# Optimization experiments

Measured on AMD Instinct MI355X. Metric: run time of the kernel, lower is better.

The kernel has to match this reference:

```python
import jax, jax.numpy as jnp
import numpy as np
from functools import partial

T, N, E, F_IN, H, F_OUT, L = 12, 20000, 320000, 128, 256, 128, 2


def _agg(feat, src, dst, n):
    # copy_u('x','m') + sum('m','h_N'): for each dst node, sum src-node features
    return jax.ops.segment_sum(feat[src], dst, num_segments=n)


def setup_inputs() -> dict:
    key = jax.random.key(0)
    ks = jax.random.split(key, 16)
    sc = 0.05
    inp = {
        "x": jax.random.normal(ks[0], (T, N, F_IN), jnp.float32),
        "h0": jax.random.normal(ks[1], (L, N, H), jnp.float32),
        "src": jax.random.randint(ks[2], (E,), 0, N, jnp.int32),
        "dst": jax.random.randint(ks[3], (E,), 0, N, jnp.int32),
        # layer 0: x-nets map F_IN->H, h-nets map H->H; stacked [r, u, c]
        "Wx0": jax.random.normal(ks[4], (3, F_IN, H), jnp.float32) * sc,
        "bx0": jnp.zeros((3, H), jnp.float32),
        "Wh0": jax.random.normal(ks[5], (3, H, H), jnp.float32) * sc,
        "bh0": jnp.zeros((3, H), jnp.float32),
        # layer 1: both map H->H
        "Wx1": jax.random.normal(ks[6], (3, H, H), jnp.float32) * sc,
        "bx1": jnp.zeros((3, H), jnp.float32),
        "Wh1": jax.random.normal(ks[7], (3, H, H), jnp.float32) * sc,
        "bh1": jnp.zeros((3, H), jnp.float32),
        "Wo": jax.random.normal(ks[8], (H, F_OUT), jnp.float32) * sc,
        "bo": jnp.zeros((F_OUT,), jnp.float32),
    }
    return inp


def _gru_cell(x_agg, h, Wx, bx, Wh, bh, src, dst, n):
    # reuse_msg_passing=True: h_agg computed once, shared by r_h_net and u_h_net
    h_agg = _agg(h, src, dst, n)
    r = jax.nn.sigmoid(x_agg @ Wx[0] + bx[0] + h_agg @ Wh[0] + bh[0])
    u = jax.nn.sigmoid(x_agg @ Wx[1] + bx[1] + h_agg @ Wh[1] + bh[1])
    # c_h_net runs on r*h, so it needs its own aggregation
    c = jnp.tanh(x_agg @ Wx[2] + bx[2] + _agg(r * h, src, dst, n) @ Wh[2] + bh[2])
    return u * h + (1.0 - u) * c


def reference(x, h0, src, dst, Wx0, bx0, Wh0, bh0, Wx1, bx1, Wh1, bh1, Wo, bo):
    n = h0.shape[1]
    # merge_time_steps=True: aggregate all time steps of x in one pass
    x_aggs = jax.vmap(lambda xi: _agg(xi, src, dst, n))(x)  # [T, N, F_IN]

    def step(carry, x_agg_t):
        h_0, h_1 = carry
        nh0 = _gru_cell(x_agg_t, h_0, Wx0, bx0, Wh0, bh0, src, dst, n)
        nh1 = _gru_cell(_agg(nh0, src, dst, n), h_1, Wx1, bx1, Wh1, bh1, src, dst, n)
        return (nh0, nh1), nh1 @ Wo + bo

    (hf0, hf1), outputs = jax.lax.scan(step, (h0[0], h0[1]), x_aggs)
    return outputs, jnp.stack([hf0, hf1])  # [T,N,F_OUT], [L,N,H]
```

## Files before the change

kernel.cpp:

```cpp
#include <hip/hip_runtime.h>
#include <hip/hip_bf16.h>
#include <stdint.h>

#define T_STEPS 12
#define NN 20000
#define NE 320000
#define FIN 128
#define HD 256
#define FOUT 128
#define PADR 96

typedef __attribute__((ext_vector_type(4))) float f32x4;
typedef __attribute__((ext_vector_type(8))) _Float16 f16x8;

static __device__ __forceinline__ float sigmoidf_(float x) {
  return 1.0f / (1.0f + __expf(-x));
}
static __device__ __forceinline__ ushort f2h(float f) {
  union { ushort s; _Float16 h; } v; v.h = (_Float16)f; return v.s;
}

static __device__ __forceinline__ void gload_lds16(const _Float16* g, _Float16* l) {
  auto gp = (const __attribute__((address_space(1))) _Float16*)g;
  auto lp = (__attribute__((address_space(3))) _Float16*)l;
  __builtin_amdgcn_global_load_lds(gp, lp, 16, 0, 0);
}

__global__ void count_kernel(const int* __restrict__ dst, int* __restrict__ counts) {
  int e = blockIdx.x * blockDim.x + threadIdx.x;
  if (e < NE) atomicAdd(&counts[dst[e]], 1);
}

__global__ void scan_kernel(const int* __restrict__ counts, int* __restrict__ offs,
                            int* __restrict__ cursor) {
  __shared__ int sm[1024];
  __shared__ int carry_s;
  if (threadIdx.x == 0) carry_s = 0;
  __syncthreads();
  const int n = NN;
  int nch = (n + 1023) >> 10;
  for (int c = 0; c < nch; ++c) {
    int i = (c << 10) + (int)threadIdx.x;
    int v = (i < n) ? counts[i] : 0;
    sm[threadIdx.x] = v;
    __syncthreads();
    for (int off = 1; off < 1024; off <<= 1) {
      int t = (threadIdx.x >= (unsigned)off) ? sm[threadIdx.x - off] : 0;
      __syncthreads();
      sm[threadIdx.x] += t;
      __syncthreads();
    }
    int incl = sm[threadIdx.x];
    int carry_local = carry_s;
    if (i < n) {
      int excl = carry_local + incl - v;
      offs[i] = excl;
      cursor[i] = excl;
    }
    __syncthreads();
    if (threadIdx.x == 1023) carry_s = carry_local + incl;
    __syncthreads();
  }
  if (threadIdx.x == 0) offs[n] = carry_s;
}

__global__ void fill_kernel(const int* __restrict__ src, const int* __restrict__ dst,
                            int* __restrict__ cursor, int* __restrict__ esrc) {
  int e = blockIdx.x * blockDim.x + threadIdx.x;
  if (e < NE) {
    int d = dst[e];
    int pos = atomicAdd(&cursor[d], 1);
    esrc[pos] = src[e];
  }
}

static __device__ __forceinline__ void agg_body256(int blk, const float* __restrict__ feat,
                                                   const int* __restrict__ offs,
                                                   const int* __restrict__ esrc,
                                                   _Float16* __restrict__ out) {
  int d = blk * 4 + (threadIdx.x >> 6);
  int lane = threadIdx.x & 63;
  int beg = offs[d], end = offs[d + 1];
  float a[8][4] = {};
  int e = beg;
  for (; e + 7 < end; e += 8) {
#pragma unroll
    for (int u = 0; u < 8; ++u) {
      float4 v = *reinterpret_cast<const float4*>(feat + (size_t)esrc[e + u] * 256 + lane * 4);
      a[u][0] += v.x; a[u][1] += v.y; a[u][2] += v.z; a[u][3] += v.w;
    }
  }
  for (; e + 3 < end; e += 4) {
#pragma unroll
    for (int u = 0; u < 4; ++u) {
      float4 v = *reinterpret_cast<const float4*>(feat + (size_t)esrc[e + u] * 256 + lane * 4);
      a[u][0] += v.x; a[u][1] += v.y; a[u][2] += v.z; a[u][3] += v.w;
    }
  }
  for (; e < end; ++e) {
    float4 v = *reinterpret_cast<const float4*>(feat + (size_t)esrc[e] * 256 + lane * 4);
    a[0][0] += v.x; a[0][1] += v.y; a[0][2] += v.z; a[0][3] += v.w;
  }
  ushort hi[4], lo[4];
#pragma unroll
  for (int p = 0; p < 4; ++p) {
    float s = ((a[0][p] + a[1][p]) + (a[2][p] + a[3][p])) +
              ((a[4][p] + a[5][p]) + (a[6][p] + a[7][p]));
    hi[p] = f2h(s);
    union { ushort us; _Float16 h; } u; u.us = hi[p];
    lo[p] = f2h(s - (float)u.h);
  }
  *reinterpret_cast<ushort4*>(out + (size_t)d * 512 + lane * 4) = *reinterpret_cast<ushort4*>(hi);
  *reinterpret_cast<ushort4*>(out + (size_t)d * 512 + 256 + lane * 4) = *reinterpret_cast<ushort4*>(lo);
}

__global__ void agg_split_h(const float* __restrict__ feat, const int* __restrict__ offs,
                            const int* __restrict__ esrc, _Float16* __restrict__ out) {
  agg_body256(blockIdx.x, feat, offs, esrc, out);
}

__global__ void agg_dual(const float* __restrict__ f0, _Float16* __restrict__ o0,
                         const float* __restrict__ f1, _Float16* __restrict__ o1,
                         const int* __restrict__ offs, const int* __restrict__ esrc) {
  if (blockIdx.y == 0) agg_body256(blockIdx.x, f0, offs, esrc, o0);
  else                 agg_body256(blockIdx.x, f1, offs, esrc, o1);
}

__global__ void agg_split_x(const float* __restrict__ x, const int* __restrict__ offs,
                            const int* __restrict__ esrc, _Float16* __restrict__ out) {
  int t = blockIdx.y;
  const float* feat = x + (size_t)t * NN * FIN;
  _Float16* o = out + (size_t)t * NN * 256;
  int d = blockIdx.x * 4 + (threadIdx.x >> 6);
  int lane = threadIdx.x & 63;
  int beg = offs[d], end = offs[d + 1];
  float a[8][2] = {};
  int e = beg;
  for (; e + 7 < end; e += 8) {
#pragma unroll
    for (int u = 0; u < 8; ++u) {
      float2 v = *reinterpret_cast<const float2*>(feat + (size_t)esrc[e + u] * FIN + lane * 2);
      a[u][0] += v.x; a[u][1] += v.y;
    }
  }
  for (; e + 3 < end; e += 4) {
#pragma unroll
    for (int u = 0; u < 4; ++u) {
      float2 v = *reinterpret_cast<const float2*>(feat + (size_t)esrc[e + u] * FIN + lane * 2);
      a[u][0] += v.x; a[u][1] += v.y;
    }
  }
  for (; e < end; ++e) {
    float2 v = *reinterpret_cast<const float2*>(feat + (size_t)esrc[e] * FIN + lane * 2);
    a[0][0] += v.x; a[0][1] += v.y;
  }
  float s0 = ((a[0][0] + a[1][0]) + (a[2][0] + a[3][0])) +
             ((a[4][0] + a[5][0]) + (a[6][0] + a[7][0]));
  float s1 = ((a[0][1] + a[1][1]) + (a[2][1] + a[3][1])) +
             ((a[4][1] + a[5][1]) + (a[6][1] + a[7][1]));
  ushort2 hi, lo;
  hi.x = f2h(s0); hi.y = f2h(s1);
  union { ushort s; _Float16 h; } u0, u1;
  u0.s = hi.x; u1.s = hi.y;
  lo.x = f2h(s0 - (float)u0.h); lo.y = f2h(s1 - (float)u1.h);
  *reinterpret_cast<ushort2*>(o + (size_t)d * 256 + lane * 2) = hi;
  *reinterpret_cast<ushort2*>(o + (size_t)d * 256 + FIN + lane * 2) = lo;
}

struct GemmP {
  const _Float16* Aa; int lda_a, wrapA, lenA;
  const _Float16* Ab; int lda_b, wrapB;
  const _Float16* B; int ldb;
  float* C; int ldc;
  const float* bias;
  const float* Cacc;
  int M, K, mode;
  float* h; _Float16* hf; float* rh;
  int nch, rpg;
};

static __device__ __forceinline__ void gemm_body(int p, const GemmP& g,
                                                 _Float16* As, _Float16* Bs) {
  int xcd = p & 7;
  int q = p >> 3;
  int rowt = xcd * g.rpg + q / g.nch;
  int chunk = q % g.nch;
  int m0 = rowt * 128;
  if (m0 >= g.M) return;
  int n0 = chunk * 128;

  int tid = threadIdx.x;
  int wave = tid >> 6;
  int lane = tid & 63;
  int wm = wave >> 1, wn = wave & 1;
  int lrow = lane & 15;
  int kgrp = lane >> 4;

  f32x4 acc[4][4] = {};

  int row8 = lane >> 3;
  int swz8 = 8 * ((lane & 7) ^ row8);
  int wrow = wave * 32;

  for (int k0 = 0; k0 < g.K; k0 += 64) {
    const _Float16* Abase;
    int ka, ldA;
    if (k0 < g.lenA) {
      ka = (k0 >= g.wrapA) ? k0 - g.wrapA : k0;
      Abase = g.Aa; ldA = g.lda_a;
    } else {
      int kp = k0 - g.lenA;
      ka = (kp >= g.wrapB) ? kp - g.wrapB : kp;
      Abase = g.Ab; ldA = g.lda_b;
    }
    __syncthreads();
#pragma unroll
    for (int p4 = 0; p4 < 4; ++p4) {
      int r = wrow + p4 * 8;
      gload_lds16(&Abase[(size_t)(m0 + r + row8) * ldA + ka + swz8], &As[r * 64]);
      gload_lds16(&g.B[(size_t)(n0 + r + row8) * g.ldb + k0 + swz8], &Bs[r * 64]);
    }
    __syncthreads();

#pragma unroll
    for (int kk = 0; kk < 2; ++kk) {
      f16x8 af[4], bf[4];
      int kbyte = kk * 64 + kgrp * 16;
#pragma unroll
      for (int i = 0; i < 4; ++i) {
        int ar = wm * 64 + i * 16 + lrow;
        af[i] = *reinterpret_cast<const f16x8*>(
            reinterpret_cast<const char*>(As) + ar * 128 + (kbyte ^ ((ar & 7) << 4)));
        int br = wn * 64 + i * 16 + lrow;
        bf[i] = *reinterpret_cast<const f16x8*>(
            reinterpret_cast<const char*>(Bs) + br * 128 + (kbyte ^ ((br & 7) << 4)));
      }
#pragma unroll
      for (int i = 0; i < 4; ++i)
#pragma unroll
        for (int j = 0; j < 4; ++j)
          acc[i][j] = __builtin_amdgcn_mfma_f32_16x16x32_f16(bf[j], af[i], acc[i][j], 0, 0, 0);
    }
  }

#pragma unroll
  for (int i = 0; i < 4; ++i) {
    int m = m0 + wm * 64 + i * 16 + lrow;
    if (m >= g.M) continue;
#pragma unroll
    for (int j = 0; j < 4; ++j) {
      int colbase = n0 + wn * 64 + j * 16 + kgrp * 4;
      f32x4 v = acc[i][j];
      if (g.mode == 0) {
        float4 bv4 = *reinterpret_cast<const float4*>(&g.bias[colbase]);
        v[0] += bv4.x; v[1] += bv4.y; v[2] += bv4.z; v[3] += bv4.w;
        *reinterpret_cast<f32x4*>(&g.C[(size_t)m * g.ldc + colbase]) = v;
      } else if (g.mode == 1) {
        if (g.Cacc) {
          float4 a4 = *reinterpret_cast<const float4*>(&g.Cacc[(size_t)m * g.ldc + colbase]);
          v[0] += a4.x; v[1] += a4.y; v[2] += a4.z; v[3] += a4.w;
        } else {
          float4 bv4 = *reinterpret_cast<const float4*>(&g.bias[colbase]);
          v[0] += bv4.x; v[1] += bv4.y; v[2] += bv4.z; v[3] += bv4.w;
        }
        if (colbase < 256) {
          float4 hv = *reinterpret_cast<const float4*>(&g.h[(size_t)m * 256 + colbase]);
          f32x4 rv;
          rv[0] = sigmoidf_(v[0]) * hv.x;
          rv[1] = sigmoidf_(v[1]) * hv.y;
          rv[2] = sigmoidf_(v[2]) * hv.z;
          rv[3] = sigmoidf_(v[3]) * hv.w;
          *reinterpret_cast<f32x4*>(&g.rh[(size_t)m * 256 + colbase]) = rv;
        } else if (colbase < 512) {
          v[0] = sigmoidf_(v[0]); v[1] = sigmoidf_(v[1]);
          v[2] = sigmoidf_(v[2]); v[3] = sigmoidf_(v[3]);
          *reinterpret_cast<f32x4*>(&g.C[(size_t)m * g.ldc + colbase]) = v;
        } else {
          *reinterpret_cast<f32x4*>(&g.C[(size_t)m * g.ldc + colbase]) = v;
        }
      } else {
        float4 xc = *reinterpret_cast<const float4*>(&g.C[(size_t)m * g.ldc + 512 + colbase]);
        float4 uu = *reinterpret_cast<const float4*>(&g.C[(size_t)m * g.ldc + 256 + colbase]);
        float* hp = &g.h[(size_t)m * 256 + colbase];
        float4 hv = *reinterpret_cast<const float4*>(hp);
        float4 nh;
        nh.x = uu.x * hv.x + (1.f - uu.x) * tanhf(xc.x + v[0]);
        nh.y = uu.y * hv.y + (1.f - uu.y) * tanhf(xc.y + v[1]);
        nh.z = uu.z * hv.z + (1.f - uu.z) * tanhf(xc.z + v[2]);
        nh.w = uu.w * hv.w + (1.f - uu.w) * tanhf(xc.w + v[3]);
        *reinterpret_cast<float4*>(hp) = nh;
        if (g.hf) {
          ushort4 hv16;
          hv16.x = f2h(nh.x); hv16.y = f2h(nh.y);
          hv16.z = f2h(nh.z); hv16.w = f2h(nh.w);
          *reinterpret_cast<ushort4*>(&g.hf[(size_t)m * 256 + colbase]) = hv16;
        }
      }
    }
  }
}

__global__ __launch_bounds__(256) void combo(GemmP ga, int na, GemmP gb, int nb, GemmP gc) {
  __shared__ _Float16 As[128 * 64];
  __shared__ _Float16 Bs[128 * 64];
  int b = blockIdx.x;
  int sel = (b < na) ? 0 : ((b < na + nb) ? 1 : 2);
  int idx = b - ((sel > 0) ? na : 0) - ((sel > 1) ? nb : 0);
  GemmP g = (sel == 0) ? ga : ((sel == 1) ? gb : gc);
  gemm_body(idx, g, As, Bs);
}

__global__ void wtrans(const float* __restrict__ W, _Float16* __restrict__ dst,
                       int K, int ldw, int ldd, int koff, int mode) {
  int k = blockIdx.x * blockDim.x + threadIdx.x;
  int n = blockIdx.y;
  if (k < K) {
    float w = W[(size_t)k * ldw + n];
    _Float16 hi = (_Float16)w;
    dst[(size_t)n * ldd + koff + k] = mode ? (_Float16)(w - (float)hi) : hi;
  }
}

__global__ void bias_comb(const float* __restrict__ bx, const float* __restrict__ bh,
                          float* __restrict__ out) {
  int i = blockIdx.x * blockDim.x + threadIdx.x;
  if (i < 768) out[i] = bx[i] + bh[i];
}

__global__ void copy_kernel(const float* __restrict__ in, float* __restrict__ out, int n4) {
  int i = blockIdx.x * blockDim.x + threadIdx.x;
  if (i < n4) reinterpret_cast<float4*>(out)[i] = reinterpret_cast<const float4*>(in)[i];
}

extern "C" void kernel_launch(void* const* d_in, const int* in_sizes, int n_in,
                              void* d_out, int out_size, void* d_ws, size_t ws_size,
                              hipStream_t stream) {
  const float* x   = (const float*)d_in[0];
  const float* h0  = (const float*)d_in[1];
  const int*   src = (const int*)d_in[2];
  const int*   dst = (const int*)d_in[3];
  const float* Wx0 = (const float*)d_in[4];
  const float* bx0 = (const float*)d_in[5];
  const float* Wh0 = (const float*)d_in[6];
  const float* bh0 = (const float*)d_in[7];
  const float* Wx1 = (const float*)d_in[8];
  const float* bx1 = (const float*)d_in[9];
  const float* Wh1 = (const float*)d_in[10];
  const float* bh1 = (const float*)d_in[11];
  const float* Wo  = (const float*)d_in[12];
  const float* bo  = (const float*)d_in[13];
  float* out = (float*)d_out;

  char* p = (char*)d_ws;
  auto alloc = [&](size_t bytes) {
    char* r = p;
    p += (bytes + 255) & ~(size_t)255;
    return r;
  };
  int* offs   = (int*)alloc((NN + 1) * sizeof(int));
  int* cursor = (int*)alloc(NN * sizeof(int));
  int* counts = (int*)alloc(NN * sizeof(int));
  int* esrc   = (int*)alloc(NE * sizeof(int));
  _Float16* B0  = (_Float16*)alloc((size_t)768 * 1152 * 2);
  _Float16* B0h = (_Float16*)alloc((size_t)256 * 768 * 2);
  _Float16* B1  = (_Float16*)alloc((size_t)768 * 1536 * 2);
  _Float16* B1h = (_Float16*)alloc((size_t)256 * 768 * 2);
  _Float16* Bo  = (_Float16*)alloc((size_t)128 * 256 * 2);
  float* b0c  = (float*)alloc(768 * 4);
  float* b1c  = (float*)alloc(768 * 4);
  _Float16* XAGG  = (_Float16*)alloc(((size_t)T_STEPS * NN + PADR) * 256 * 2);
  _Float16* H0AGG = (_Float16*)alloc((size_t)(NN + PADR) * 512 * 2);
  _Float16* H1AGG = (_Float16*)alloc((size_t)(NN + PADR) * 512 * 2);
  _Float16* RHAGG = (_Float16*)alloc((size_t)(NN + PADR) * 512 * 2);
  _Float16* h1f   = (_Float16*)alloc((size_t)(NN + PADR) * 256 * 2);
  float* rhf  = (float*)alloc((size_t)NN * 256 * 4);
  float* xw0  = (float*)alloc((size_t)NN * 768 * 4);
  float* xw1  = (float*)alloc((size_t)NN * 768 * 4);

  float* h0c = out + (size_t)T_STEPS * NN * FOUT;
  float* h1c = h0c + (size_t)NN * HD;

  hipMemsetAsync(counts, 0, NN * sizeof(int), stream);
  count_kernel<<<(NE + 255) / 256, 256, 0, stream>>>(dst, counts);
  scan_kernel<<<1, 1024, 0, stream>>>(counts, offs, cursor);
  fill_kernel<<<(NE + 255) / 256, 256, 0, stream>>>(src, dst, cursor, esrc);

  hipMemsetAsync(B0, 0, (size_t)768 * 1152 * 2, stream);
  hipMemsetAsync(B1, 0, (size_t)768 * 1536 * 2, stream);
  for (int g = 0; g < 3; ++g) {
    const float* W = Wx0 + (size_t)g * 128 * 256;
    _Float16* D = B0 + (size_t)g * 256 * 1152;
    wtrans<<<dim3(1, 256), 256, 0, stream>>>(W, D, 128, 256, 1152, 0, 0);
    wtrans<<<dim3(1, 256), 256, 0, stream>>>(W, D, 128, 256, 1152, 128, 0);
    wtrans<<<dim3(1, 256), 256, 0, stream>>>(W, D, 128, 256, 1152, 256, 1);
  }
  for (int g = 0; g < 2; ++g) {
    const float* W = Wh0 + (size_t)g * 256 * 256;
    _Float16* D = B0 + (size_t)g * 256 * 1152;
    wtrans<<<dim3(1, 256), 256, 0, stream>>>(W, D, 256, 256, 1152, 384, 0);
    wtrans<<<dim3(1, 256), 256, 0, stream>>>(W, D, 256, 256, 1152, 640, 0);
    wtrans<<<dim3(1, 256), 256, 0, stream>>>(W, D, 256, 256, 1152, 896, 1);
  }
  {
    const float* W = Wh0 + (size_t)2 * 256 * 256;
    wtrans<<<dim3(1, 256), 256, 0, stream>>>(W, B0h, 256, 256, 768, 0, 0);
    wtrans<<<dim3(1, 256), 256, 0, stream>>>(W, B0h, 256, 256, 768, 256, 0);
    wtrans<<<dim3(1, 256), 256, 0, stream>>>(W, B0h, 256, 256, 768, 512, 1);
  }
  for (int g = 0; g < 3; ++g) {
    const float* W = Wx1 + (size_t)g * 256 * 256;
    _Float16* D = B1 + (size_t)g * 256 * 1536;
    wtrans<<<dim3(1, 256), 256, 0, stream>>>(W, D, 256, 256, 1536, 0, 0);
    wtrans<<<dim3(1, 256), 256, 0, stream>>>(W, D, 256, 256, 1536, 256, 0);
    wtrans<<<dim3(1, 256), 256, 0, stream>>>(W, D, 256, 256, 1536, 512, 1);
  }
  for (int g = 0; g < 2; ++g) {
    const float* W = Wh1 + (size_t)g * 256 * 256;
    _Float16* D = B1 + (size_t)g * 256 * 1536;
    wtrans<<<dim3(1, 256), 256, 0, stream>>>(W, D, 256, 256, 1536, 768, 0);
    wtrans<<<dim3(1, 256), 256, 0, stream>>>(W, D, 256, 256, 1536, 1024, 0);
    wtrans<<<dim3(1, 256), 256, 0, stream>>>(W, D, 256, 256, 1536, 1280, 1);
  }
  {
    const float* W = Wh1 + (size_t)2 * 256 * 256;
    wtrans<<<dim3(1, 256), 256, 0, stream>>>(W, B1h, 256, 256, 768, 0, 0);
    wtrans<<<dim3(1, 256), 256, 0, stream>>>(W, B1h, 256, 256, 768, 256, 0);
    wtrans<<<dim3(1, 256), 256, 0, stream>>>(W, B1h, 256, 256, 768, 512, 1);
  }
  wtrans<<<dim3(1, 128), 256, 0, stream>>>(Wo, Bo, 256, 128, 256, 0, 0);
  bias_comb<<<3, 256, 0, stream>>>(bx0, bh0, b0c);
  bias_comb<<<3, 256, 0, stream>>>(bx1, bh1, b1c);

  copy_kernel<<<(2 * NN * HD / 4 + 255) / 256, 256, 0, stream>>>(h0, h0c, 2 * NN * HD / 4);

  dim3 blk(256);
  const int RPG = 20;
  int g6 = 8 * RPG * 6, g2 = 8 * RPG * 2, g1 = 8 * RPG * 1;
  int agg_grid = NN / 4;

  agg_split_x<<<dim3(agg_grid, T_STEPS), blk, 0, stream>>>(x, offs, esrc, XAGG);
  agg_split_h<<<agg_grid, blk, 0, stream>>>(h0c, offs, esrc, H0AGG);

  GemmP dummy = {};
  dummy.nch = 1; dummy.rpg = 1;

  for (int t = 0; t < T_STEPS; ++t) {
    GemmP C1p = {RHAGG, 512, 512, 768, nullptr, 0, 0, B1h, 768, xw1, 768, nullptr, nullptr,
                 NN, 768, 2, h1c, h1f, nullptr, 2, RPG};
    GemmP L0p = {XAGG + (size_t)t * NN * 256, 256, 256, 384, H0AGG, 512, 512,
                 B0, 1152, xw0, 768, b0c, nullptr, NN, 1152, 1, h0c, nullptr, rhf, 6, RPG};
    if (t == 0)
      combo<<<g6, blk, 0, stream>>>(L0p, g6, dummy, 0, dummy);
    else
      combo<<<g2 + g6, blk, 0, stream>>>(C1p, g2, L0p, g6, dummy);

    agg_dual<<<dim3(agg_grid, 2), blk, 0, stream>>>(rhf, RHAGG, h1c, H1AGG, offs, esrc);

    GemmP C0p = {RHAGG, 512, 512, 768, nullptr, 0, 0, B0h, 768, xw0, 768, nullptr, nullptr,
                 NN, 768, 2, h0c, nullptr, nullptr, 2, RPG};
    GemmP L1a = {H1AGG, 512, 512, 768, nullptr, 0, 0, B1 + 768, 1536, xw1, 768, b1c, nullptr,
                 NN, 768, 0, nullptr, nullptr, nullptr, 6, RPG};
    GemmP OPp = {h1f, 256, 256, 256, nullptr, 0, 0, Bo, 256,
                 out + (size_t)(t > 0 ? t - 1 : 0) * NN * FOUT, FOUT, bo, nullptr,
                 NN, 256, 0, nullptr, nullptr, nullptr, 1, RPG};
    if (t == 0)
      combo<<<g2 + g6, blk, 0, stream>>>(C0p, g2, L1a, g6, dummy);
    else
      combo<<<g2 + g6 + g1, blk, 0, stream>>>(C0p, g2, L1a, g6, OPp);

    agg_split_h<<<agg_grid, blk, 0, stream>>>(h0c, offs, esrc, H0AGG);

    GemmP L1b = {H0AGG, 512, 512, 768, nullptr, 0, 0, B1, 1536, xw1, 768, nullptr, xw1,
                 NN, 768, 1, h1c, nullptr, rhf, 6, RPG};
    combo<<<g6, blk, 0, stream>>>(L1b, g6, dummy, 0, dummy);

    agg_split_h<<<agg_grid, blk, 0, stream>>>(rhf, offs, esrc, RHAGG);
  }

  GemmP C1f = {RHAGG, 512, 512, 768, nullptr, 0, 0, B1h, 768, xw1, 768, nullptr, nullptr,
               NN, 768, 2, h1c, h1f, nullptr, 2, RPG};
  combo<<<g2, blk, 0, stream>>>(C1f, g2, dummy, 0, dummy);
  GemmP OPl = {h1f, 256, 256, 256, nullptr, 0, 0, Bo, 256,
               out + (size_t)(T_STEPS - 1) * NN * FOUT, FOUT, bo, nullptr,
               NN, 256, 0, nullptr, nullptr, nullptr, 1, RPG};
  combo<<<g1, blk, 0, stream>>>(OPl, g1, dummy, 0, dummy);
}
```

Before: 4.968 ms.

## Scalarize edge indices, use fast tanh, and move output GEMM to L1b launch

The gather loops now load edge source indices through readfirstlane, so the compiler can treat them as wave-uniform scalars and use scalar address arithmetic. The GRU update replaces tanhf with an exp-based fast tanh. The output-projection GEMM blocks for the previous step move from the C0/L1a launch into the L1b launch, which rebalances work across the fused launches. The fast tanh changes numerics slightly, and for large arguments the exp can overflow to inf, which still yields the correct limit.

```diff
diff --git a/kernel.cpp b/kernel.cpp
--- a/kernel.cpp
+++ b/kernel.cpp
@@ -15,6 +15,9 @@
 
 static __device__ __forceinline__ float sigmoidf_(float x) {
   return 1.0f / (1.0f + __expf(-x));
+}
+static __device__ __forceinline__ float tanhf_(float x) {
+  return 1.0f - 2.0f / (__expf(2.0f * x) + 1.0f);
 }
 static __device__ __forceinline__ ushort f2h(float f) {
   union { ushort s; _Float16 h; } v; v.h = (_Float16)f; return v.s;
@@ -84,21 +87,28 @@
   float a[8][4] = {};
   int e = beg;
   for (; e + 7 < end; e += 8) {
+    int s[8];
+#pragma unroll
+    for (int u = 0; u < 8; ++u) s[u] = __builtin_amdgcn_readfirstlane(esrc[e + u]);
 #pragma unroll
     for (int u = 0; u < 8; ++u) {
-      float4 v = *reinterpret_cast<const float4*>(feat + (size_t)esrc[e + u] * 256 + lane * 4);
+      float4 v = *reinterpret_cast<const float4*>(feat + (size_t)s[u] * 256 + lane * 4);
       a[u][0] += v.x; a[u][1] += v.y; a[u][2] += v.z; a[u][3] += v.w;
     }
   }
   for (; e + 3 < end; e += 4) {
+    int s[4];
+#pragma unroll
+    for (int u = 0; u < 4; ++u) s[u] = __builtin_amdgcn_readfirstlane(esrc[e + u]);
 #pragma unroll
     for (int u = 0; u < 4; ++u) {
-      float4 v = *reinterpret_cast<const float4*>(feat + (size_t)esrc[e + u] * 256 + lane * 4);
+      float4 v = *reinterpret_cast<const float4*>(feat + (size_t)s[u] * 256 + lane * 4);
       a[u][0] += v.x; a[u][1] += v.y; a[u][2] += v.z; a[u][3] += v.w;
     }
   }
   for (; e < end; ++e) {
-    float4 v = *reinterpret_cast<const float4*>(feat + (size_t)esrc[e] * 256 + lane * 4);
+    int s0 = __builtin_amdgcn_readfirstlane(esrc[e]);
+    float4 v = *reinterpret_cast<const float4*>(feat + (size_t)s0 * 256 + lane * 4);
     a[0][0] += v.x; a[0][1] += v.y; a[0][2] += v.z; a[0][3] += v.w;
   }
   ushort hi[4], lo[4];
@@ -137,21 +147,28 @@
   float a[8][2] = {};
   int e = beg;
   for (; e + 7 < end; e += 8) {
+    int s[8];
+#pragma unroll
+    for (int u = 0; u < 8; ++u) s[u] = __builtin_amdgcn_readfirstlane(esrc[e + u]);
 #pragma unroll
     for (int u = 0; u < 8; ++u) {
-      float2 v = *reinterpret_cast<const float2*>(feat + (size_t)esrc[e + u] * FIN + lane * 2);
+      float2 v = *reinterpret_cast<const float2*>(feat + (size_t)s[u] * FIN + lane * 2);
       a[u][0] += v.x; a[u][1] += v.y;
     }
   }
   for (; e + 3 < end; e += 4) {
+    int s[4];
+#pragma unroll
+    for (int u = 0; u < 4; ++u) s[u] = __builtin_amdgcn_readfirstlane(esrc[e + u]);
 #pragma unroll
     for (int u = 0; u < 4; ++u) {
-      float2 v = *reinterpret_cast<const float2*>(feat + (size_t)esrc[e + u] * FIN + lane * 2);
+      float2 v = *reinterpret_cast<const float2*>(feat + (size_t)s[u] * FIN + lane * 2);
       a[u][0] += v.x; a[u][1] += v.y;
     }
   }
   for (; e < end; ++e) {
-    float2 v = *reinterpret_cast<const float2*>(feat + (size_t)esrc[e] * FIN + lane * 2);
+    int s0 = __builtin_amdgcn_readfirstlane(esrc[e]);
+    float2 v = *reinterpret_cast<const float2*>(feat + (size_t)s0 * FIN + lane * 2);
     a[0][0] += v.x; a[0][1] += v.y;
   }
   float s0 = ((a[0][0] + a[1][0]) + (a[2][0] + a[3][0])) +
@@ -284,10 +301,10 @@
         float* hp = &g.h[(size_t)m * 256 + colbase];
         float4 hv = *reinterpret_cast<const float4*>(hp);
         float4 nh;
-        nh.x = uu.x * hv.x + (1.f - uu.x) * tanhf(xc.x + v[0]);
-        nh.y = uu.y * hv.y + (1.f - uu.y) * tanhf(xc.y + v[1]);
-        nh.z = uu.z * hv.z + (1.f - uu.z) * tanhf(xc.z + v[2]);
-        nh.w = uu.w * hv.w + (1.f - uu.w) * tanhf(xc.w + v[3]);
+        nh.x = uu.x * hv.x + (1.f - uu.x) * tanhf_(xc.x + v[0]);
+        nh.y = uu.y * hv.y + (1.f - uu.y) * tanhf_(xc.y + v[1]);
+        nh.z = uu.z * hv.z + (1.f - uu.z) * tanhf_(xc.z + v[2]);
+        nh.w = uu.w * hv.w + (1.f - uu.w) * tanhf_(xc.w + v[3]);
         *reinterpret_cast<float4*>(hp) = nh;
         if (g.hf) {
           ushort4 hv16;
@@ -460,19 +477,19 @@
                  NN, 768, 2, h0c, nullptr, nullptr, 2, RPG};
     GemmP L1a = {H1AGG, 512, 512, 768, nullptr, 0, 0, B1 + 768, 1536, xw1, 768, b1c, nullptr,
                  NN, 768, 0, nullptr, nullptr, nullptr, 6, RPG};
+    combo<<<g2 + g6, blk, 0, stream>>>(C0p, g2, L1a, g6, dummy);
+
+    agg_split_h<<<agg_grid, blk, 0, stream>>>(h0c, offs, esrc, H0AGG);
+
+    GemmP L1b = {H0AGG, 512, 512, 768, nullptr, 0, 0, B1, 1536, xw1, 768, nullptr, xw1,
+                 NN, 768, 1, h1c, nullptr, rhf, 6, RPG};
     GemmP OPp = {h1f, 256, 256, 256, nullptr, 0, 0, Bo, 256,
                  out + (size_t)(t > 0 ? t - 1 : 0) * NN * FOUT, FOUT, bo, nullptr,
                  NN, 256, 0, nullptr, nullptr, nullptr, 1, RPG};
     if (t == 0)
-      combo<<<g2 + g6, blk, 0, stream>>>(C0p, g2, L1a, g6, dummy);
+      combo<<<g6, blk, 0, stream>>>(L1b, g6, dummy, 0, dummy);
     else
-      combo<<<g2 + g6 + g1, blk, 0, stream>>>(C0p, g2, L1a, g6, OPp);
-
-    agg_split_h<<<agg_grid, blk, 0, stream>>>(h0c, offs, esrc, H0AGG);
-
-    GemmP L1b = {H0AGG, 512, 512, 768, nullptr, 0, 0, B1, 1536, xw1, 768, nullptr, xw1,
-                 NN, 768, 1, h1c, nullptr, rhf, 6, RPG};
-    combo<<<g6, blk, 0, stream>>>(L1b, g6, dummy, 0, dummy);
+      combo<<<g6 + g1, blk, 0, stream>>>(L1b, g6, OPp, g1, dummy);
 
     agg_split_h<<<agg_grid, blk, 0, stream>>>(rhf, offs, esrc, RHAGG);
   }
```

Result: faster. 4.813 ms (-3.1%).
